# Kernel tuning notes

Measured on AMD Instinct MI355X. Metric: run time of the kernel, lower is better.

The kernel has to match this reference:

```python
import jax, jax.numpy as jnp
import numpy as np

B, C, H, W = 4, 256, 48, 48
HEADS, DH = 8, 64
HID = HEADS * DH
EPS = 1e-5
SCALE = DH ** -0.5


def setup_inputs() -> dict:
    key = jax.random.key(0)
    ks = jax.random.split(key, 8)
    return {
        "tensor": jax.random.normal(ks[0], (B, C, H, W), jnp.float32),
        "norm_g": jnp.ones((C,), jnp.float32),                      # ChanLayerNorm gamma
        "w_qkv": jax.random.normal(ks[1], (3 * HID, C), jnp.float32) * 0.02,  # 1x1 conv, no bias
        "dw_q": jax.random.normal(ks[2], (HID, 1, 3, 3), jnp.float32) * 0.1,  # depthwise 3x3
        "dw_k": jax.random.normal(ks[3], (HID, 1, 3, 3), jnp.float32) * 0.1,
        "dw_v": jax.random.normal(ks[4], (HID, 1, 3, 3), jnp.float32) * 0.1,
        "w_out": jax.random.normal(ks[5], (C, HID), jnp.float32) * 0.02,      # 1x1 conv out
        "b_out": jnp.zeros((C,), jnp.float32),
    }


def _rope(t):
    # t: (b, h, s, d) -- rotary embedding over flattened spatial positions
    s, d = t.shape[-2], t.shape[-1]
    inv_freq = 1.0 / (10000.0 ** (jnp.arange(0, d, 2, dtype=jnp.float32) / d))
    freqs = jnp.arange(s, dtype=jnp.float32)[:, None] * inv_freq[None, :]     # (s, d/2)
    emb = jnp.concatenate([freqs, freqs], axis=-1)                            # (s, d)
    cos, sin = jnp.cos(emb), jnp.sin(emb)
    t1, t2 = t[..., : d // 2], t[..., d // 2 :]
    rot = jnp.concatenate([-t2, t1], axis=-1)
    return t * cos + rot * sin


def _dwconv(x, w):
    # depthwise 3x3, padding=1 (Primer conv), groups = channels
    return jax.lax.conv_general_dilated(
        x, w, window_strides=(1, 1), padding="SAME",
        feature_group_count=x.shape[1],
        dimension_numbers=("NCHW", "OIHW", "NCHW"))


def reference(tensor, norm_g, w_qkv, dw_q, dw_k, dw_v, w_out, b_out):
    x = tensor
    # ChanLayerNorm: normalize over channel dim
    mean = jnp.mean(x, axis=1, keepdims=True)
    var = jnp.var(x, axis=1, keepdims=True)
    xn = (x - mean) * jax.lax.rsqrt(var + EPS) * norm_g[None, :, None, None]
    # 1x1 conv to qkv
    qkv = jnp.einsum("bchw,oc->bohw", xn, w_qkv)
    q, k, v = jnp.split(qkv, 3, axis=1)
    q, k, v = _dwconv(q, dw_q), _dwconv(k, dw_k), _dwconv(v, dw_v)
    # b (h d) x y -> b h (x y) d
    def to_seq(t):
        b = t.shape[0]
        return t.reshape(b, HEADS, DH, H * W).transpose(0, 1, 3, 2)
    q, k, v = to_seq(q), to_seq(k), to_seq(v)
    q, k = _rope(q), _rope(k)
    q = q * SCALE
    sim = jnp.einsum("bhid,bhjd->bhij", q, k)
    attn = jax.nn.softmax(sim, axis=-1)
    out = jnp.einsum("bhij,bhjd->bhid", attn, v)
    # b h (x y) d -> b (h d) x y
    out = out.transpose(0, 1, 3, 2).reshape(out.shape[0], HID, H, W)
    return jnp.einsum("bchw,oc->bohw", out, w_out) + b_out[None, :, None, None]
```

## Files before the change

### kernel.cpp

```cpp
#include <hip/hip_runtime.h>
#include <math.h>

#define SS 2304
#define C_IN 256
#define HID 512
#define QKV3 1536
#define HEADS 8
#define DH 64
#define BATCH 4
#define EPSV 1e-5f
#define SCALEV_LOG2E 0.18033688011112042f

typedef short s8v __attribute__((ext_vector_type(8)));
typedef float f4v __attribute__((ext_vector_type(4)));
typedef unsigned int u4v __attribute__((ext_vector_type(4)));
typedef unsigned int uint32;

static __device__ inline unsigned short f2bf(float x) {
    unsigned int u = __float_as_uint(x);
    u += 0x7fffu + ((u >> 16) & 1u);
    return (unsigned short)(u >> 16);
}
static __device__ inline float bf2f(unsigned short h) {
    return __uint_as_float((unsigned int)h << 16);
}
static __device__ inline f4v mm(s8v a, s8v b, f4v c) {
    return __builtin_amdgcn_mfma_f32_16x16x32_bf16(a, b, c, 0, 0, 0);
}
static __device__ inline s8v pk4(uint32 a, uint32 b, uint32 c, uint32 d) {
    u4v t; t[0] = a; t[1] = b; t[2] = c; t[3] = d;
    return __builtin_bit_cast(s8v, t);
}
static __device__ inline uint32 pk_rnd(float x) {
    unsigned int u = __float_as_uint(x);
    unsigned int uh = (u + (0x7fffu + ((u >> 16) & 1u))) & 0xffff0000u;
    float r = x - __uint_as_float(uh);
#if __has_builtin(__builtin_amdgcn_perm)
    return __builtin_amdgcn_perm(__float_as_uint(r), uh, 0x07060302u);
#else
    return (uh >> 16) | (__float_as_uint(r) & 0xffff0000u);
#endif
}
static __device__ inline uint32 pk_trunc(float x) {
    unsigned int u = __float_as_uint(x);
    unsigned int h = u & 0xffff0000u;
    float r = x - __uint_as_float(h);
#if __has_builtin(__builtin_amdgcn_perm)
    return __builtin_amdgcn_perm(__float_as_uint(r), u, 0x07060302u);
#else
    return (h >> 16) | (__float_as_uint(r) & 0xffff0000u);
#endif
}
static __device__ inline float unpk(uint32 u) {
    return __uint_as_float(u << 16) + __uint_as_float(u & 0xffff0000u);
}
static __device__ inline uint32 rot16(uint32 u) { return (u >> 16) | (u << 16); }
static __device__ inline u4v rot16v(u4v u) {
    u4v r; r[0] = rot16(u[0]); r[1] = rot16(u[1]); r[2] = rot16(u[2]); r[3] = rot16(u[3]);
    return r;
}

__global__ void prep_all(const float* __restrict__ w_qkv, const float* __restrict__ g,
                         uint32* __restrict__ wgint, float* __restrict__ wsum,
                         const float* __restrict__ w_out, uint32* __restrict__ woutint,
                         float* __restrict__ cosT, float* __restrict__ sinT) {
    __shared__ float red[256];
    int bid = blockIdx.x;
    int t = threadIdx.x;
    if (bid < QKV3) {
        int o = bid, c = t;
        float v = w_qkv[o * C_IN + c] * g[c];
        wgint[o * C_IN + c] = pk_rnd(v);
        red[c] = v;
        __syncthreads();
        for (int st = 128; st > 0; st >>= 1) {
            if (c < st) red[c] += red[c + st];
            __syncthreads();
        }
        if (c == 0) wsum[o] = red[0];
    } else if (bid < QKV3 + 512) {
        int idx = (bid - QKV3) * 256 + t;
        woutint[idx] = pk_rnd(w_out[idx]);
    } else {
        int idx = (bid - QKV3 - 512) * 256 + t;
        int s = idx >> 5, f = idx & 31;
        double inv = pow(10000.0, -(double)f / 32.0);
        double ang = (double)s * inv;
        cosT[idx] = (float)cos(ang);
        sinT[idx] = (float)sin(ang);
    }
}

__global__ __launch_bounds__(256) void xt_pack(const float* __restrict__ x,
                                               uint32* __restrict__ xTint,
                                               float* __restrict__ psum,
                                               float* __restrict__ psq) {
    __shared__ float tile[64][65];
    __shared__ float sred[4][64];
    __shared__ float qred[4][64];
    int b = blockIdx.z;
    int c0 = blockIdx.y * 64;
    int s0 = blockIdx.x * 64;
    int t = threadIdx.x;
    int sl = t & 63, cg = t >> 6;
    float ps = 0.f, pq = 0.f;
#pragma unroll
    for (int i = 0; i < 16; ++i) {
        int c = cg * 16 + i;
        float v = x[((size_t)b * C_IN + c0 + c) * SS + s0 + sl];
        tile[c][sl] = v;
        ps += v;
        pq += v * v;
    }
    sred[cg][sl] = ps;
    qred[cg][sl] = pq;
    __syncthreads();
    int cl = t & 63, sg = t >> 6;
#pragma unroll
    for (int i = 0; i < 16; ++i) {
        int s = sg * 16 + i;
        xTint[((size_t)b * SS + s0 + s) * C_IN + c0 + cl] = pk_rnd(tile[cl][s]);
    }
    if (t < 64) {
        float S = (sred[0][t] + sred[1][t]) + (sred[2][t] + sred[3][t]);
        float Q = (qred[0][t] + qred[1][t]) + (qred[2][t] + qred[3][t]);
        size_t o = (size_t)blockIdx.y * (BATCH * SS) + (size_t)b * SS + s0 + t;
        psum[o] = S;
        psq[o] = Q;
    }
}

__global__ __launch_bounds__(256, 4) void qkv_mfma(
    const uint32* __restrict__ wgint, const uint32* __restrict__ xTint,
    const float* __restrict__ wsum, const float* __restrict__ psum,
    const float* __restrict__ psq, uint32* __restrict__ qkvint) {
    int b = blockIdx.z;
    int m0 = blockIdx.y * 128;
    int n0 = blockIdx.x * 64;
    int t = threadIdx.x;
    int wv = t >> 6, lane = t & 63, l15 = lane & 15, quad = lane >> 4;
    int wm = wv * 32;
    const uint32* Ab = wgint + (size_t)(m0 + wm) * C_IN;
    const uint32* Bb = xTint + ((size_t)b * SS + n0) * C_IN;
    f4v acc[2][4];
#pragma unroll
    for (int mt = 0; mt < 2; ++mt)
#pragma unroll
        for (int nt = 0; nt < 4; ++nt) acc[mt][nt] = (f4v){0.f, 0.f, 0.f, 0.f};
    u4v af[2][2], bf[2][4];
    auto ldA = [&](int ch, u4v* A) {
#pragma unroll
        for (int mt = 0; mt < 2; ++mt)
            A[mt] = *(const u4v*)(Ab + (size_t)(mt * 16 + l15) * C_IN + ch * 16 + quad * 4);
    };
    auto ldB = [&](int ch, u4v* B) {
#pragma unroll
        for (int nt = 0; nt < 4; ++nt)
            B[nt] = *(const u4v*)(Bb + (size_t)(nt * 16 + l15) * C_IN + ch * 16 + quad * 4);
    };
    ldA(0, af[0]);
    ldB(0, bf[0]);
#pragma unroll 2
    for (int ch = 0; ch < 16; ++ch) {
        int cur = ch & 1, nxt = cur ^ 1;
        if (ch + 1 < 16) { ldA(ch + 1, af[nxt]); ldB(ch + 1, bf[nxt]); }
        u4v br[4];
#pragma unroll
        for (int nt = 0; nt < 4; ++nt) br[nt] = rot16v(bf[cur][nt]);
#pragma unroll
        for (int mt = 0; mt < 2; ++mt) {
            s8v a = __builtin_bit_cast(s8v, af[cur][mt]);
#pragma unroll
            for (int nt = 0; nt < 4; ++nt) {
                acc[mt][nt] = mm(a, __builtin_bit_cast(s8v, bf[cur][nt]), acc[mt][nt]);
                acc[mt][nt] = mm(a, __builtin_bit_cast(s8v, br[nt]), acc[mt][nt]);
            }
        }
    }
    const int NP = BATCH * SS;
    float mnv[4], rsv[4];
#pragma unroll
    for (int nt = 0; nt < 4; ++nt) {
        int p = b * SS + n0 + nt * 16 + l15;
        float S = (psum[p] + psum[NP + p]) + (psum[2 * NP + p] + psum[3 * NP + p]);
        float Q = (psq[p] + psq[NP + p]) + (psq[2 * NP + p] + psq[3 * NP + p]);
        float mu = S * (1.0f / C_IN);
        mnv[nt] = mu;
        rsv[nt] = rsqrtf(Q * (1.0f / C_IN) - mu * mu + EPSV);
    }
#pragma unroll
    for (int mt = 0; mt < 2; ++mt)
#pragma unroll
        for (int r = 0; r < 4; ++r) {
            int m = m0 + wm + mt * 16 + quad * 4 + r;
            float ws = wsum[m];
            uint32* dst = qkvint + ((size_t)b * QKV3 + m) * SS + n0 + l15;
#pragma unroll
            for (int nt = 0; nt < 4; ++nt)
                dst[nt * 16] = pk_rnd(rsv[nt] * (acc[mt][nt][r] - mnv[nt] * ws));
        }
}

__global__ __launch_bounds__(256) void conv_rope(
    const uint32* __restrict__ qkvint, const float* __restrict__ dwq,
    const float* __restrict__ dwk, const float* __restrict__ dwv,
    const float* __restrict__ cosT, const float* __restrict__ sinT,
    unsigned short* __restrict__ qhi, unsigned short* __restrict__ qlo,
    unsigned short* __restrict__ khi, unsigned short* __restrict__ klo,
    uint32* __restrict__ vtint) {
    __shared__ float tile[64][65];
    int b = blockIdx.z;
    int part = blockIdx.y >> 3;
    int h = blockIdx.y & 7;
    int s0 = blockIdx.x * 64;
    int t = threadIdx.x;
    int sl = t & 63, dgrp = t >> 6;
    int s = s0 + sl;
    int y = s / 48, xx = s - y * 48;
    int bh = b * HEADS + h;
    const float* dw = (part == 0) ? dwq : (part == 1) ? dwk : dwv;
#pragma unroll
    for (int i = 0; i < 16; ++i) {
        int d = dgrp * 16 + i;
        int cch = part * HID + h * DH + d;
        const uint32* src = qkvint + ((size_t)b * QKV3 + cch) * SS;
        const float* wp = dw + (h * DH + d) * 9;
        float acc = 0.f;
#pragma unroll
        for (int dy = -1; dy <= 1; ++dy) {
            int yy = y + dy;
            if (yy < 0 || yy >= 48) continue;
#pragma unroll
            for (int dx = -1; dx <= 1; ++dx) {
                int xv = xx + dx;
                if (xv < 0 || xv >= 48) continue;
                acc += wp[(dy + 1) * 3 + (dx + 1)] * unpk(src[yy * 48 + xv]);
            }
        }
        if (part == 2) {
            size_t o = ((size_t)bh * DH + d) * SS + s;
            vtint[o] = pk_rnd(acc);
        } else {
            tile[d][sl] = acc;
        }
    }
    if (part == 2) return;
    __syncthreads();
    int d2 = t & 63, srow = t >> 6;
    unsigned short* hiA = (part == 0) ? qhi : khi;
    unsigned short* loA = (part == 0) ? qlo : klo;
#pragma unroll
    for (int i = 0; i < 16; ++i) {
        int sp = srow + 4 * i;
        float v0 = tile[d2][sp];
        float vp = tile[d2 ^ 32][sp];
        int f = d2 & 31;
        float cv = cosT[(s0 + sp) * 32 + f];
        float sv = sinT[(s0 + sp) * 32 + f];
        float rot = (d2 < 32) ? -vp : vp;
        float val = v0 * cv + rot * sv;
        if (part == 0) val *= SCALEV_LOG2E;
        size_t o = ((size_t)bh * SS + s0 + sp) * DH + d2;
        unsigned short hu = f2bf(val);
        hiA[o] = hu;
        loA[o] = f2bf(val - bf2f(hu));
    }
}

__global__ __launch_bounds__(256, 2) void attn_mfma(
    const unsigned short* __restrict__ qhi, const unsigned short* __restrict__ qlo,
    const unsigned short* __restrict__ khi, const unsigned short* __restrict__ klo,
    const uint32* __restrict__ vtint, uint32* __restrict__ OTint) {
    __shared__ float lds[2][64][67];
    __shared__ float lsl[4][64];
    int n = blockIdx.y * 36 + blockIdx.x;
    int xcd = n & 7, slot = n >> 3;
    int bh = (xcd << 2) | (slot / 36);
    int i0 = (slot % 36) * 64;
    int t = threadIdx.x;
    int wv = t >> 6;
    int lane = t & 63;
    int l15 = lane & 15;
    int quad = lane >> 4;

    {
        char* qw = (char*)lds;
#pragma unroll
        for (int r = 0; r < 4; ++r) {
            int idx = r * 256 + t;
            int o = idx & 7;
            int q = (idx >> 3) & 63;
            int p = idx >> 9;
            const unsigned short* src =
                (p ? qlo : qhi) + ((size_t)bh * SS + i0 + q) * DH + o * 8;
            *(s8v*)(qw + p * 8192 + o * 1024 + q * 16) = *(const s8v*)src;
        }
    }
    __syncthreads();
    const char* qrd = (const char*)lds;
    const int qoff = l15 * 16 + quad * 1024;

    f4v oacc[4][4];
#pragma unroll
    for (int dt = 0; dt < 4; ++dt)
#pragma unroll
        for (int ig = 0; ig < 4; ++ig) oacc[dt][ig] = (f4v){0.f, 0.f, 0.f, 0.f};
    float lsum[4] = {0.f, 0.f, 0.f, 0.f};

    const size_t kbh = (size_t)bh * SS * DH;
    const uint32* vbase = vtint + (size_t)bh * DH * SS;
    const int jbase = wv * 16;

    s8v kc[2][4], vc[4];
    auto ldK = [&](int s, s8v* K) {
        size_t row = kbh + (size_t)(jbase + s * 64 + l15) * DH + quad * 8;
        K[0] = *(const s8v*)(khi + row);
        K[1] = *(const s8v*)(khi + row + 32);
        K[2] = *(const s8v*)(klo + row);
        K[3] = *(const s8v*)(klo + row + 32);
    };
    auto ldV = [&](int s, s8v* V) {
        size_t col = (size_t)(jbase + s * 64 + quad * 4);
#pragma unroll
        for (int dt = 0; dt < 4; ++dt)
            V[dt] = __builtin_bit_cast(
                s8v, *(const u4v*)(vbase + (size_t)(dt * 16 + l15) * SS + col));
    };
    ldK(0, kc[0]);
#pragma unroll 2
    for (int s = 0; s < 36; ++s) {
        int cur = s & 1, nxt = cur ^ 1;
        ldV(s, vc);
        if (s + 1 < 36) { ldK(s + 1, kc[nxt]); }
#pragma unroll
        for (int ig = 0; ig < 4; ++ig) {
            s8v q0 = *(const s8v*)(qrd + (qoff + ig * 256));
            s8v q1 = *(const s8v*)(qrd + (qoff + ig * 256 + 4096));
            s8v q2 = *(const s8v*)(qrd + (qoff + ig * 256 + 8192));
            s8v q3 = *(const s8v*)(qrd + (qoff + ig * 256 + 12288));
            f4v sx = {0.f, 0.f, 0.f, 0.f};
            sx = mm(kc[cur][0], q0, sx);
            sx = mm(kc[cur][1], q1, sx);
            sx = mm(kc[cur][0], q2, sx);
            sx = mm(kc[cur][1], q3, sx);
            sx = mm(kc[cur][2], q0, sx);
            sx = mm(kc[cur][3], q1, sx);
            float p0 = __builtin_amdgcn_exp2f(sx[0]);
            float p1 = __builtin_amdgcn_exp2f(sx[1]);
            float p2 = __builtin_amdgcn_exp2f(sx[2]);
            float p3 = __builtin_amdgcn_exp2f(sx[3]);
            lsum[ig] += (p0 + p1) + (p2 + p3);
            uint32 u0 = pk_trunc(p0), u1 = pk_trunc(p1);
            uint32 u2 = pk_trunc(p2), u3 = pk_trunc(p3);
            s8v B1 = pk4(u0, u1, u2, u3);
            s8v B2 = pk4(rot16(u0), rot16(u1), rot16(u2), rot16(u3));
#pragma unroll
            for (int dt = 0; dt < 4; ++dt) {
                oacc[dt][ig] = mm(vc[dt], B1, oacc[dt][ig]);
                oacc[dt][ig] = mm(vc[dt], B2, oacc[dt][ig]);
            }
        }
    }
#pragma unroll
    for (int ig = 0; ig < 4; ++ig) {
        float v = lsum[ig];
        v += __shfl_xor(v, 16);
        v += __shfl_xor(v, 32);
        if (quad == 0) lsl[wv][ig * 16 + l15] = v;
    }
    __syncthreads();
    if (wv < 2) {
#pragma unroll
        for (int dt = 0; dt < 4; ++dt)
#pragma unroll
            for (int ig = 0; ig < 4; ++ig)
#pragma unroll
                for (int r = 0; r < 4; ++r)
                    lds[wv][dt * 16 + quad * 4 + r][ig * 16 + l15] = oacc[dt][ig][r];
    }
    __syncthreads();
    if (wv >= 2) {
#pragma unroll
        for (int dt = 0; dt < 4; ++dt)
#pragma unroll
            for (int ig = 0; ig < 4; ++ig)
#pragma unroll
                for (int r = 0; r < 4; ++r)
                    lds[wv - 2][dt * 16 + quad * 4 + r][ig * 16 + l15] += oacc[dt][ig][r];
    }
    __syncthreads();
    int q = t >> 2, dg = t & 3;
    float linv = 1.f / ((lsl[0][q] + lsl[1][q]) + (lsl[2][q] + lsl[3][q]));
    int b = bh >> 3, h = bh & 7;
    uint32* dst = OTint + ((size_t)b * SS + i0 + q) * HID + h * DH + dg * 16;
    u4v ov[4];
#pragma unroll
    for (int j4 = 0; j4 < 4; ++j4)
#pragma unroll
        for (int i = 0; i < 4; ++i) {
            int d = dg * 16 + j4 * 4 + i;
            ov[j4][i] = pk_rnd((lds[0][d][q] + lds[1][d][q]) * linv);
        }
#pragma unroll
    for (int j4 = 0; j4 < 4; ++j4) *(u4v*)(dst + j4 * 4) = ov[j4];
}

__global__ __launch_bounds__(256, 4) void outproj_mfma(
    const uint32* __restrict__ OTint, const uint32* __restrict__ woutint,
    const float* __restrict__ b_out, float* __restrict__ out) {
    int b = blockIdx.z;
    int m0 = blockIdx.y * 32;
    int n0 = blockIdx.x * 128;
    int t = threadIdx.x;
    int wv = t >> 6, lane = t & 63, l15 = lane & 15, quad = lane >> 4;
    int wn = wv * 32;
    const uint32* Ab = woutint + (size_t)m0 * HID;
    const uint32* Bb = OTint + ((size_t)b * SS + n0 + wn) * HID;
    f4v acc[2][2];
#pragma unroll
    for (int mt = 0; mt < 2; ++mt)
#pragma unroll
        for (int nt = 0; nt < 2; ++nt) acc[mt][nt] = (f4v){0.f, 0.f, 0.f, 0.f};
    u4v af[2][2], bf[2][2];
    auto ldA = [&](int ch, u4v* A) {
#pragma unroll
        for (int mt = 0; mt < 2; ++mt)
            A[mt] = *(const u4v*)(Ab + (size_t)(mt * 16 + l15) * HID + ch * 16 + quad * 4);
    };
    auto ldB = [&](int ch, u4v* B) {
#pragma unroll
        for (int nt = 0; nt < 2; ++nt)
            B[nt] = *(const u4v*)(Bb + (size_t)(nt * 16 + l15) * HID + ch * 16 + quad * 4);
    };
    ldA(0, af[0]);
    ldB(0, bf[0]);
#pragma unroll 2
    for (int ch = 0; ch < 32; ++ch) {
        int cur = ch & 1, nxt = cur ^ 1;
        if (ch + 1 < 32) { ldA(ch + 1, af[nxt]); ldB(ch + 1, bf[nxt]); }
        u4v br[2];
#pragma unroll
        for (int nt = 0; nt < 2; ++nt) br[nt] = rot16v(bf[cur][nt]);
#pragma unroll
        for (int mt = 0; mt < 2; ++mt) {
            s8v a = __builtin_bit_cast(s8v, af[cur][mt]);
#pragma unroll
            for (int nt = 0; nt < 2; ++nt) {
                acc[mt][nt] = mm(a, __builtin_bit_cast(s8v, bf[cur][nt]), acc[mt][nt]);
                acc[mt][nt] = mm(a, __builtin_bit_cast(s8v, br[nt]), acc[mt][nt]);
            }
        }
    }
#pragma unroll
    for (int mt = 0; mt < 2; ++mt)
#pragma unroll
        for (int r = 0; r < 4; ++r) {
            int o = m0 + mt * 16 + quad * 4 + r;
            float bo = b_out[o];
            float* dst = out + ((size_t)b * C_IN + o) * SS + n0 + wn + l15;
#pragma unroll
            for (int nt = 0; nt < 2; ++nt) dst[nt * 16] = acc[mt][nt][r] + bo;
        }
}

extern "C" void kernel_launch(void* const* d_in, const int* in_sizes, int n_in,
                              void* d_out, int out_size, void* d_ws, size_t ws_size,
                              hipStream_t stream) {
    (void)in_sizes; (void)n_in; (void)out_size; (void)ws_size;
    const float* x     = (const float*)d_in[0];
    const float* g     = (const float*)d_in[1];
    const float* w_qkv = (const float*)d_in[2];
    const float* dwq   = (const float*)d_in[3];
    const float* dwk   = (const float*)d_in[4];
    const float* dwv   = (const float*)d_in[5];
    const float* w_out = (const float*)d_in[6];
    const float* b_out = (const float*)d_in[7];
    float* out = (float*)d_out;

    char* ws = (char*)d_ws;
    size_t off = 0;
    auto alloc = [&](size_t nbytes) -> void* {
        char* p = ws + off;
        off = (off + nbytes + 255) & ~(size_t)255;
        return (void*)p;
    };
    const size_t NSD = (size_t)BATCH * HEADS * SS * DH;
    uint32* wgint   = (uint32*)alloc((size_t)QKV3 * C_IN * 4);
    uint32* woutint = (uint32*)alloc((size_t)C_IN * HID * 4);
    float* wsum = (float*)alloc((size_t)QKV3 * 4);
    float* psum = (float*)alloc((size_t)4 * BATCH * SS * 4);
    float* psq  = (float*)alloc((size_t)4 * BATCH * SS * 4);
    float* cosT = (float*)alloc((size_t)SS * 32 * 4);
    float* sinT = (float*)alloc((size_t)SS * 32 * 4);
    char* scratchA = (char*)alloc((size_t)3 * NSD * 4);
    unsigned short* qhi  = (unsigned short*)alloc(NSD * 2);
    unsigned short* qlo  = (unsigned short*)alloc(NSD * 2);
    unsigned short* khi  = (unsigned short*)alloc(NSD * 2);
    unsigned short* klo  = (unsigned short*)alloc(NSD * 2);
    uint32* vtint = (uint32*)alloc(NSD * 4);
    uint32* xTint  = (uint32*)qhi;
    uint32* qkvint = (uint32*)scratchA;
    uint32* OTint  = (uint32*)scratchA;

    prep_all<<<QKV3 + 512 + 288, 256, 0, stream>>>(w_qkv, g, wgint, wsum,
                                                   w_out, woutint, cosT, sinT);
    xt_pack<<<dim3(36, 4, BATCH), 256, 0, stream>>>(x, xTint, psum, psq);
    qkv_mfma<<<dim3(36, 12, BATCH), 256, 0, stream>>>(wgint, xTint, wsum, psum, psq,
                                                      qkvint);
    conv_rope<<<dim3(36, 24, BATCH), 256, 0, stream>>>(qkvint, dwq, dwk, dwv, cosT, sinT,
                                                       qhi, qlo, khi, klo, vtint);
    attn_mfma<<<dim3(36, 32), 256, 0, stream>>>(qhi, qlo, khi, klo, vtint, OTint);
    outproj_mfma<<<dim3(18, 8, BATCH), 256, 0, stream>>>(OTint, woutint, b_out, out);
}
```

Measured before the change: 472.2 us.

## Drop K double buffer, split QK and PV phases, raise attention occupancy to 3

Replaces the two-slot K register double buffer with a single slot. All four QK^T score tiles are computed first and kept in registers, then the next K tile is loaded while the exp/PV phase runs. Launch bounds go from 2 to 3 blocks per SIMD to fit more waves and hide latency. The trade-off is a tighter register budget that could cause spills, plus a shorter window for the K prefetch to overlap.

```diff
diff --git a/kernel.cpp b/kernel.cpp
--- a/kernel.cpp
+++ b/kernel.cpp
@@ -267,7 +267,7 @@
     }
 }
 
-__global__ __launch_bounds__(256, 2) void attn_mfma(
+__global__ __launch_bounds__(256, 3) void attn_mfma(
     const unsigned short* __restrict__ qhi, const unsigned short* __restrict__ qlo,
     const unsigned short* __restrict__ khi, const unsigned short* __restrict__ klo,
     const uint32* __restrict__ vtint, uint32* __restrict__ OTint) {
@@ -311,7 +311,7 @@
     const uint32* vbase = vtint + (size_t)bh * DH * SS;
     const int jbase = wv * 16;
 
-    s8v kc[2][4], vc[4];
+    s8v kc[4], vc[4];
     auto ldK = [&](int s, s8v* K) {
         size_t row = kbh + (size_t)(jbase + s * 64 + l15) * DH + quad * 8;
         K[0] = *(const s8v*)(khi + row);
@@ -326,12 +326,11 @@
             V[dt] = __builtin_bit_cast(
                 s8v, *(const u4v*)(vbase + (size_t)(dt * 16 + l15) * SS + col));
     };
-    ldK(0, kc[0]);
+    ldK(0, kc);
 #pragma unroll 2
     for (int s = 0; s < 36; ++s) {
-        int cur = s & 1, nxt = cur ^ 1;
         ldV(s, vc);
-        if (s + 1 < 36) { ldK(s + 1, kc[nxt]); }
+        f4v sv[4];
 #pragma unroll
         for (int ig = 0; ig < 4; ++ig) {
             s8v q0 = *(const s8v*)(qrd + (qoff + ig * 256));
@@ -339,16 +338,21 @@
             s8v q2 = *(const s8v*)(qrd + (qoff + ig * 256 + 8192));
             s8v q3 = *(const s8v*)(qrd + (qoff + ig * 256 + 12288));
             f4v sx = {0.f, 0.f, 0.f, 0.f};
-            sx = mm(kc[cur][0], q0, sx);
-            sx = mm(kc[cur][1], q1, sx);
-            sx = mm(kc[cur][0], q2, sx);
-            sx = mm(kc[cur][1], q3, sx);
-            sx = mm(kc[cur][2], q0, sx);
-            sx = mm(kc[cur][3], q1, sx);
-            float p0 = __builtin_amdgcn_exp2f(sx[0]);
-            float p1 = __builtin_amdgcn_exp2f(sx[1]);
-            float p2 = __builtin_amdgcn_exp2f(sx[2]);
-            float p3 = __builtin_amdgcn_exp2f(sx[3]);
+            sx = mm(kc[0], q0, sx);
+            sx = mm(kc[1], q1, sx);
+            sx = mm(kc[0], q2, sx);
+            sx = mm(kc[1], q3, sx);
+            sx = mm(kc[2], q0, sx);
+            sx = mm(kc[3], q1, sx);
+            sv[ig] = sx;
+        }
+        if (s + 1 < 36) ldK(s + 1, kc);
+#pragma unroll
+        for (int ig = 0; ig < 4; ++ig) {
+            float p0 = __builtin_amdgcn_exp2f(sv[ig][0]);
+            float p1 = __builtin_amdgcn_exp2f(sv[ig][1]);
+            float p2 = __builtin_amdgcn_exp2f(sv[ig][2]);
+            float p3 = __builtin_amdgcn_exp2f(sv[ig][3]);
             lsum[ig] += (p0 + p1) + (p2 + p3);
             uint32 u0 = pk_trunc(p0), u1 = pk_trunc(p1);
             uint32 u2 = pk_trunc(p2), u3 = pk_trunc(p3);
```

New measurement: 794.1 us. 1.68x slower.
